# Kernel optimization log

Hardware: AMD Instinct MI355X
Metric: run time of the kernel (lower is better)

Reference implementation:

```python
import jax, jax.numpy as jnp
import numpy as np
import math

B, S, E = 4, 2048, 1024
H, KV = 16, 4            # query heads, kv heads
HD = E // H              # head_dim = 64
R, CD = 8, 64            # TPA rank, context dim
NQ, NL = 8, 2            # qubits, VQC layers
EPS = 1e-6
LN_EPS = 1e-5


def setup_inputs() -> dict:
    key = jax.random.key(0)
    ks = jax.random.split(key, 16)
    def dense(k, i, o):
        return (jax.random.normal(k, (i, o), jnp.float32) / np.float32(np.sqrt(i)))
    d = {}
    d["x"] = jax.random.normal(ks[0], (B, S, E), jnp.float32)
    d["ctxW"] = dense(ks[1], E, CD);      d["ctxb"] = jnp.zeros((CD,), jnp.float32)
    d["qaW"] = dense(ks[2], E, R * HD);   d["qab"] = jnp.zeros((R * HD,), jnp.float32)
    d["qbW"] = dense(ks[3], CD, R * H);   d["qbb"] = jnp.zeros((R * H,), jnp.float32)
    d["kaW"] = dense(ks[4], E, R * HD);   d["kab"] = jnp.zeros((R * HD,), jnp.float32)
    d["kbW"] = dense(ks[5], CD, R * KV);  d["kbb"] = jnp.zeros((R * KV,), jnp.float32)
    d["vaW"] = dense(ks[6], E, R * HD);   d["vab"] = jnp.zeros((R * HD,), jnp.float32)
    d["vbW"] = dense(ks[7], CD, R * KV);  d["vbb"] = jnp.zeros((R * KV,), jnp.float32)
    d["qeW"] = dense(ks[8], HD, NQ);      d["qeb"] = jnp.zeros((NQ,), jnp.float32)
    d["vqc"] = jax.random.normal(ks[9], (NL, NQ, 3), jnp.float32) * 0.3
    d["ent"] = jnp.array([0.1], jnp.float32)
    d["outW"] = dense(ks[10], E, E);      d["outb"] = jnp.zeros((E,), jnp.float32)
    d["gamma"] = jnp.ones((E,), jnp.float32)
    d["beta"] = jnp.zeros((E,), jnp.float32)
    return d


def _tpa(x, ctx, aW, ab, bW, bb, nh):
    # output = sum_r (x @ A_r) outer (ctx @ B_r)  ->  [b, nh, s, head_dim]
    b, s, _ = x.shape
    a = (x @ aW + ab).reshape(b, s, R, HD)
    bf = (ctx @ bW + bb).reshape(b, s, R, nh)
    return jnp.einsum('bsrd,bsrh->bhsd', a, bf)


def _quantum_features(x, qeW, qeb, vqc, ent):
    # x: [b, h, s, HD] -> features [b, h, s, 2*NQ]
    angles = jnp.tanh(x @ qeW + qeb) * math.pi
    f = angles
    for l in range(NL):
        p = vqc[l]  # [NQ, 3]
        f = jnp.cos(f + p[:, 0]) * jnp.sin(f + p[:, 1]) + jnp.cos(f + p[:, 2])
        f = f * (1.0 + ent[0] * jnp.roll(f, shift=1, axis=-1))  # entanglement
    qf = jnp.concatenate([jnp.cos(f), jnp.sin(f)], axis=-1)
    return qf / (jnp.linalg.norm(qf, axis=-1, keepdims=True) + EPS)


def reference(x, ctxW, ctxb, qaW, qab, qbW, qbb, kaW, kab, kbW, kbb,
              vaW, vab, vbW, vbb, qeW, qeb, vqc, ent, outW, outb, gamma, beta):
    ctx = x @ ctxW + ctxb                              # [B,S,CD]
    q = _tpa(x, ctx, qaW, qab, qbW, qbb, H)            # [B,H,S,HD]
    k = _tpa(x, ctx, kaW, kab, kbW, kbb, KV)           # [B,KV,S,HD]
    v = _tpa(x, ctx, vaW, vab, vbW, vbb, KV)
    # GQA: expand KV heads to match query heads
    k = jnp.repeat(k, H // KV, axis=1)
    v = jnp.repeat(v, H // KV, axis=1)
    qf = _quantum_features(q, qeW, qeb, vqc, ent)      # [B,H,S,2*NQ]
    kf = _quantum_features(k, qeW, qeb, vqc, ent)
    # causal linear attention via cumulative KV state
    kv = jnp.cumsum(jnp.einsum('bhsf,bhsd->bhsfd', kf, v), axis=2)
    num = jnp.einsum('bhsf,bhsfd->bhsd', qf, kv)
    den = jnp.einsum('bhsf,bhsf->bhs', qf, jnp.cumsum(kf, axis=2))
    attn = num / (den[..., None] + EPS)                # [B,H,S,HD]
    o = attn.transpose(0, 2, 1, 3).reshape(B, S, E) @ outW + outb
    y = x + o                                          # residual + layernorm
    mu = jnp.mean(y, axis=-1, keepdims=True)
    var = jnp.mean(jnp.square(y - mu), axis=-1, keepdims=True)
    return gamma * (y - mu) / jnp.sqrt(var + LN_EPS) + beta
```

## Files before the change

### kernel.cpp

```cpp
#include <hip/hip_runtime.h>
#include <math.h>

#define Bb  4
#define Ss  2048
#define Ee  1024
#define Hh  16
#define KVh 4
#define HD  64
#define RNK 8
#define CDd 64
#define NQ  8
#define NLn 2
#define NF  16
#define NC  32
#define CT  (Ss/NC)
#define BS  (Bb*Ss)
#define NCAT 1664

typedef unsigned short ushort_t;
typedef __attribute__((ext_vector_type(8))) short short8;
typedef __attribute__((ext_vector_type(4))) float f32x4;
typedef __attribute__((ext_vector_type(4))) unsigned short u16x4;

__device__ __forceinline__ unsigned short f2bf(float f) {
    unsigned int u = __float_as_uint(f);
    unsigned int r = (u + 0x7FFFu + ((u >> 16) & 1u)) >> 16;
    return (unsigned short)r;
}
__device__ __forceinline__ float bf2f(unsigned short h) {
    return __uint_as_float(((unsigned int)h) << 16);
}

#define GLD16(gp, lp) \
    __builtin_amdgcn_global_load_lds((const __attribute__((address_space(1))) void*)(gp), \
                                     (__attribute__((address_space(3))) void*)(lp), 16, 0, 0)

__global__ __launch_bounds__(256)
void cast_f32_bf16(const float* __restrict__ in, ushort_t* __restrict__ outp, long n)
{
    long i = ((long)blockIdx.x * blockDim.x + threadIdx.x) * 8;
    if (i >= n) return;
    short8 o;
    #pragma unroll
    for (int j = 0; j < 8; ++j) o[j] = (short)f2bf(in[i + j]);
    *(short8*)(outp + i) = o;
}

__global__ __launch_bounds__(256)
void weight_prep(const float* __restrict__ qaW, const float* __restrict__ kaW,
                 const float* __restrict__ vaW, const float* __restrict__ outW,
                 const float* __restrict__ ctxW,
                 const float* __restrict__ qab, const float* __restrict__ kab,
                 const float* __restrict__ vab, const float* __restrict__ ctxb,
                 ushort_t* __restrict__ WcatT, ushort_t* __restrict__ outWt,
                 float* __restrict__ bcat)
{
    __shared__ float t[32][33];
    const int bid = blockIdx.x;
    const int tx = threadIdx.x & 31, ty = threadIdx.x >> 5;
    if (bid < 1536) {
        const int z = bid >> 9;
        const int r = bid & 511;
        const int k0 = (r & 31) * 32, n0 = (r >> 5) * 32;
        const float* W = (z == 0) ? qaW : (z == 1) ? kaW : vaW;
        const int nOff = 512 * z;
        #pragma unroll
        for (int i = 0; i < 4; ++i)
            t[ty + 8*i][tx] = W[(size_t)(k0 + ty + 8*i) * 512 + (n0 + tx)];
        __syncthreads();
        #pragma unroll
        for (int i = 0; i < 4; ++i)
            WcatT[(size_t)(nOff + n0 + ty + 8*i) * Ee + (k0 + tx)] = f2bf(t[tx][ty + 8*i]);
    } else if (bid < 2560) {
        const int r = bid - 1536;
        const int k0 = (r & 31) * 32, n0 = (r >> 5) * 32;
        #pragma unroll
        for (int i = 0; i < 4; ++i)
            t[ty + 8*i][tx] = outW[(size_t)(k0 + ty + 8*i) * 1024 + (n0 + tx)];
        __syncthreads();
        #pragma unroll
        for (int i = 0; i < 4; ++i)
            outWt[(size_t)(n0 + ty + 8*i) * Ee + (k0 + tx)] = f2bf(t[tx][ty + 8*i]);
    } else {
        const int pid = bid - 2560;
        if (pid < 64) {
            const int k0 = (pid >> 1) * 32, n0 = (pid & 1) * 32;
            #pragma unroll
            for (int i = 0; i < 4; ++i)
                t[ty + 8*i][tx] = ctxW[(size_t)(k0 + ty + 8*i) * 64 + (n0 + tx)];
            __syncthreads();
            #pragma unroll
            for (int i = 0; i < 4; ++i)
                WcatT[(size_t)(1536 + n0 + ty + 8*i) * Ee + (k0 + tx)] = f2bf(t[tx][ty + 8*i]);
        } else if (pid < 96) {
            const int idx = (pid - 64) * 2048 + threadIdx.x * 8;
            short8 z = {0, 0, 0, 0, 0, 0, 0, 0};
            *(short8*)(WcatT + (size_t)1600 * Ee + idx) = z;
        } else {
            const int n = (pid - 96) * 256 + threadIdx.x;
            if (n < NCAT) {
                float v = 0.f;
                if      (n < 512)  v = qab[n];
                else if (n < 1024) v = kab[n - 512];
                else if (n < 1536) v = vab[n - 1024];
                else if (n < 1600) v = ctxb[n - 1536];
                bcat[n] = v;
            }
        }
    }
}

template<int RES, int OUTBF>
__global__ __launch_bounds__(256)
void gemm_mfma(const ushort_t* __restrict__ A, const ushort_t* __restrict__ Bt,
               const float* __restrict__ bias, const float* __restrict__ res,
               void* __restrict__ Cout, int M, int N, int K)
{
    __shared__ ushort_t Al[128 * 32];
    __shared__ ushort_t Bl[128 * 32];
    const int tid  = threadIdx.x;
    const int lane = tid & 63;
    const int wave = tid >> 6;
    const int wm = wave >> 1;
    const int wn = wave & 1;

    const unsigned nx  = gridDim.x;
    const unsigned bid = blockIdx.y * nx + blockIdx.x;
    const unsigned nwg = nx * gridDim.y;
    const unsigned qc = nwg >> 3, rc = nwg & 7;
    const unsigned xc = bid & 7, of = bid >> 3;
    const unsigned tile = (xc < rc ? xc * (qc + 1) : rc * (qc + 1) + (xc - rc) * qc) + of;
    const int bm = (int)(tile / nx) * 128;
    const int bn = (int)(tile % nx) * 128;

    f32x4 acc[4][4] = {};

    const int arow0 = wave * 16 + (lane >> 2);
    const int kq = lane & 3;
    const ushort_t* Ag0 = A  + (size_t)(bm + arow0) * K + kq * 8;
    const ushort_t* Ag1 = A  + (size_t)(bm + 64 + arow0) * K + kq * 8;
    const ushort_t* Bg0 = Bt + (size_t)(bn + arow0) * K + kq * 8;
    const ushort_t* Bg1 = Bt + (size_t)(bn + 64 + arow0) * K + kq * 8;
    ushort_t* Alw = Al + wave * 512;
    ushort_t* Blw = Bl + wave * 512;

    const int fr = lane & 15;
    const int fg = lane >> 4;

    for (int k0 = 0; k0 < K; k0 += 32) {
        GLD16(Ag0 + k0, Alw);
        GLD16(Ag1 + k0, Alw + 2048);
        GLD16(Bg0 + k0, Blw);
        GLD16(Bg1 + k0, Blw + 2048);
        __syncthreads();
        short8 af[4], bfv[4];
        #pragma unroll
        for (int mi = 0; mi < 4; ++mi)
            af[mi] = *(const short8*)&Al[(wm*64 + mi*16 + fr) * 32 + fg * 8];
        #pragma unroll
        for (int ni = 0; ni < 4; ++ni)
            bfv[ni] = *(const short8*)&Bl[(wn*64 + ni*16 + fr) * 32 + fg * 8];
        #pragma unroll
        for (int mi = 0; mi < 4; ++mi)
            #pragma unroll
            for (int ni = 0; ni < 4; ++ni)
                acc[mi][ni] = __builtin_amdgcn_mfma_f32_16x16x32_bf16(
                    af[mi], bfv[ni], acc[mi][ni], 0, 0, 0);
        __syncthreads();
    }

    float bv[4];
    #pragma unroll
    for (int ni = 0; ni < 4; ++ni) bv[ni] = bias[bn + wn*64 + ni*16 + fr];
    #pragma unroll
    for (int mi = 0; mi < 4; ++mi) {
        #pragma unroll
        for (int ni = 0; ni < 4; ++ni) {
            const int gn = bn + wn*64 + ni*16 + fr;
            #pragma unroll
            for (int r = 0; r < 4; ++r) {
                const int gm = bm + wm*64 + mi*16 + fg*4 + r;
                float v = acc[mi][ni][r] + bv[ni];
                if (RES) v += res[(size_t)gm * N + gn];
                if (OUTBF) ((ushort_t*)Cout)[(size_t)gm * N + gn] = f2bf(v);
                else       ((float*)Cout)[(size_t)gm * N + gn] = v;
            }
        }
    }
}

__global__ __launch_bounds__(256)
void combine_quantum(const ushort_t* __restrict__ Cf,
                     const float* __restrict__ qbW, const float* __restrict__ qbb,
                     const float* __restrict__ kbW, const float* __restrict__ kbb,
                     const float* __restrict__ vbW, const float* __restrict__ vbb,
                     const float* __restrict__ qeW, const float* __restrict__ qeb,
                     const float* __restrict__ vqc, const float* __restrict__ ent,
                     float* __restrict__ qf_g, float* __restrict__ kf_g,
                     float* __restrict__ v_g)
{
    const int wid = threadIdx.x >> 6;
    const int d   = threadIdx.x & 63;
    const int bs  = blockIdx.x * 4 + wid;
    const int b = bs >> 11;
    const int s = bs & 2047;

    __shared__ float qew_s[HD*NQ];
    __shared__ float ctx_l[4][CDd];
    __shared__ float bfq[4][128];
    __shared__ float bfk[4][32];
    __shared__ float bfv[4][32];
    __shared__ float rows[4][Hh+KVh][65];

    #pragma unroll
    for (int i = 0; i < 2; ++i)
        qew_s[threadIdx.x + 256*i] = qeW[threadIdx.x + 256*i];

    const ushort_t* Crow = Cf + (size_t)bs * NCAT;
    ctx_l[wid][d] = bf2f(Crow[1536 + d]);
    __syncthreads();

    {
        float q0 = qbb[d], q1 = qbb[d + 64];
        float kv = (d < 32) ? kbb[d] : vbb[d - 32];
        const float* Wkv = (d < 32) ? (kbW + d) : (vbW + (d - 32));
        #pragma unroll 8
        for (int k = 0; k < CDd; ++k) {
            const float c = ctx_l[wid][k];
            q0 += c * qbW[(size_t)k*128 + d];
            q1 += c * qbW[(size_t)k*128 + d + 64];
            kv += c * Wkv[(size_t)k*32];
        }
        bfq[wid][d] = q0; bfq[wid][d + 64] = q1;
        if (d < 32) bfk[wid][d] = kv; else bfv[wid][d - 32] = kv;
    }

    float aq[RNK], ak[RNK], av[RNK];
    #pragma unroll
    for (int r = 0; r < RNK; ++r) {
        aq[r] = bf2f(Crow[r*64 + d]);
        ak[r] = bf2f(Crow[512 + r*64 + d]);
        av[r] = bf2f(Crow[1024 + r*64 + d]);
    }
    __syncthreads();

    #pragma unroll
    for (int h = 0; h < Hh; ++h) {
        float acc = 0.f;
        #pragma unroll
        for (int r = 0; r < RNK; ++r) acc += aq[r] * bfq[wid][r*16 + h];
        rows[wid][h][d] = acc;
    }
    #pragma unroll
    for (int kvh = 0; kvh < KVh; ++kvh) {
        float acck = 0.f, accv = 0.f;
        #pragma unroll
        for (int r = 0; r < RNK; ++r) {
            acck += ak[r] * bfk[wid][r*4 + kvh];
            accv += av[r] * bfv[wid][r*4 + kvh];
        }
        rows[wid][Hh + kvh][d] = acck;
        v_g[((size_t)(b*KVh + kvh)*Ss + s)*HD + d] = accv;
    }
    __syncthreads();

    const float entv = ent[0];
    const int i   = d & 7;
    const int src = (d & ~7) | ((i + 7) & 7);
    float p00 = vqc[(0*NQ + i)*3 + 0], p01 = vqc[(0*NQ + i)*3 + 1], p02 = vqc[(0*NQ + i)*3 + 2];
    float p10 = vqc[(1*NQ + i)*3 + 0], p11 = vqc[(1*NQ + i)*3 + 1], p12 = vqc[(1*NQ + i)*3 + 2];
    const float qebi = qeb[i];

    #pragma unroll
    for (int stripe = 0; stripe < 3; ++stripe) {
        const int row = stripe * 8 + (d >> 3);
        const bool active = (row < Hh + KVh);
        const int rowc = active ? row : (Hh + KVh - 1);
        float acc = qebi;
        #pragma unroll 16
        for (int dd = 0; dd < HD; ++dd)
            acc += rows[wid][rowc][dd] * qew_s[dd*8 + i];
        float f = tanhf(acc) * 3.14159265358979323846f;
        float g = cosf(f + p00) * sinf(f + p01) + cosf(f + p02);
        float gp = __shfl(g, src, 64);
        f = g * (1.f + entv * gp);
        g = cosf(f + p10) * sinf(f + p11) + cosf(f + p12);
        gp = __shfl(g, src, 64);
        f = g * (1.f + entv * gp);
        float c = cosf(f), sn = sinf(f);
        float ss = c*c + sn*sn;
        ss += __shfl_xor(ss, 1, 64);
        ss += __shfl_xor(ss, 2, 64);
        ss += __shfl_xor(ss, 4, 64);
        const float inv = 1.f / (sqrtf(ss) + 1e-6f);
        if (active) {
            float* dst = (row < Hh)
                ? qf_g + ((size_t)(b*Hh + row)*Ss + s)*NF
                : kf_g + ((size_t)(b*KVh + (row - Hh))*Ss + s)*NF;
            dst[i]      = c * inv;
            dst[NQ + i] = sn * inv;
        }
    }
}

__global__ __launch_bounds__(64)
void chunk_partial(const float* __restrict__ kf_g, const float* __restrict__ v_g,
                   float* __restrict__ kvpart, float* __restrict__ kfpart)
{
    const int id = blockIdx.x;
    const int c = id & (NC-1);
    const int bk = id / NC;
    const int d = threadIdx.x;
    __shared__ float kf_l[CT][NF];
    const int s0 = c * CT;
    const float* kfp = kf_g + ((size_t)bk*Ss + s0)*NF;
    #pragma unroll
    for (int t = 0; t < (CT*NF)/64; ++t)
        ((float*)kf_l)[d + 64*t] = kfp[d + 64*t];
    __syncthreads();
    float st[NF] = {};
    const float* vp = v_g + ((size_t)bk*Ss + s0)*HD;
    for (int t = 0; t < CT; ++t) {
        const float vd = vp[(size_t)t*HD + d];
        #pragma unroll
        for (int f = 0; f < NF; ++f) st[f] += kf_l[t][f] * vd;
    }
    float* kvp = kvpart + (size_t)id * (NF*HD);
    #pragma unroll
    for (int f = 0; f < NF; ++f) kvp[f*HD + d] = st[f];
    if (d < NF) {
        float acc = 0.f;
        for (int t = 0; t < CT; ++t) acc += kf_l[t][d];
        kfpart[(size_t)id*NF + d] = acc;
    }
}

__global__ __launch_bounds__(64)
void attn_scan(const float* __restrict__ qf_g, const float* __restrict__ kf_g,
               const float* __restrict__ v_g,
               const float* __restrict__ kvpart, const float* __restrict__ kfpart,
               ushort_t* __restrict__ o_bf)
{
    const int id = blockIdx.x;
    const int c = id & (NC-1);
    const int bh = id / NC;
    const int h = bh & (Hh-1);
    const int b = bh / Hh;
    const int kvh = h >> 2;
    const int d = threadIdx.x;
    __shared__ float kf_l[CT][NF];
    __shared__ float qf_l[CT][NF];
    const int s0 = c * CT;
    const float* kfp = kf_g + ((size_t)(b*KVh + kvh)*Ss + s0)*NF;
    const float* qfp = qf_g + ((size_t)(b*Hh + h)*Ss + s0)*NF;
    #pragma unroll
    for (int t = 0; t < (CT*NF)/64; ++t) {
        ((float*)kf_l)[d + 64*t] = kfp[d + 64*t];
        ((float*)qf_l)[d + 64*t] = qfp[d + 64*t];
    }
    float st[NF] = {};
    float kfs[NF] = {};
    const int bk = b*KVh + kvh;
    for (int cc = 0; cc < c; ++cc) {
        const float* kvp = kvpart + ((size_t)bk*NC + cc)*(NF*HD);
        const float* kfq = kfpart + ((size_t)bk*NC + cc)*NF;
        #pragma unroll
        for (int f = 0; f < NF; ++f) {
            st[f]  += kvp[f*HD + d];
            kfs[f] += kfq[f];
        }
    }
    __syncthreads();
    const float* vp = v_g + ((size_t)(b*KVh + kvh)*Ss + s0)*HD;
    ushort_t* op = o_bf + ((size_t)(b*Ss + s0))*Ee + h*HD;
    for (int t = 0; t < CT; ++t) {
        const float vd = vp[(size_t)t*HD + d];
        float num0 = 0.f, num1 = 0.f, den0 = 0.f, den1 = 0.f;
        #pragma unroll
        for (int f = 0; f < NF; f += 2) {
            const float kv0 = kf_l[t][f];
            const float kv1 = kf_l[t][f+1];
            st[f]   += kv0 * vd;   kfs[f]   += kv0;
            st[f+1] += kv1 * vd;   kfs[f+1] += kv1;
            const float qv0 = qf_l[t][f];
            const float qv1 = qf_l[t][f+1];
            num0 += qv0 * st[f];   den0 += qv0 * kfs[f];
            num1 += qv1 * st[f+1]; den1 += qv1 * kfs[f+1];
        }
        op[(size_t)t*Ee + d] = f2bf((num0 + num1) / ((den0 + den1) + 1e-6f));
    }
}

__global__ __launch_bounds__(256)
void layernorm_res(const float* __restrict__ x, const ushort_t* __restrict__ o_bf,
                   const float* __restrict__ gamma, const float* __restrict__ beta,
                   float* __restrict__ out)
{
    __shared__ float tmp[4];
    const int row = blockIdx.x;
    const int t = threadIdx.x;
    const float* xp = x + (size_t)row * Ee;
    const ushort_t* op = o_bf + (size_t)row * Ee;
    const f32x4 xv = *(const f32x4*)(xp + t*4);
    const u16x4 ov = *(const u16x4*)(op + t*4);
    float v[4];
    float sum = 0.f;
    #pragma unroll
    for (int i = 0; i < 4; ++i) { v[i] = xv[i] + bf2f(ov[i]); sum += v[i]; }
    #pragma unroll
    for (int o = 32; o > 0; o >>= 1) sum += __shfl_down(sum, o, 64);
    if ((t & 63) == 0) tmp[t >> 6] = sum;
    __syncthreads();
    const float mu = (tmp[0] + tmp[1] + tmp[2] + tmp[3]) * (1.f/Ee);
    __syncthreads();
    float vs = 0.f;
    #pragma unroll
    for (int i = 0; i < 4; ++i) { const float dd = v[i] - mu; vs += dd*dd; }
    #pragma unroll
    for (int o = 32; o > 0; o >>= 1) vs += __shfl_down(vs, o, 64);
    if ((t & 63) == 0) tmp[t >> 6] = vs;
    __syncthreads();
    const float var = (tmp[0] + tmp[1] + tmp[2] + tmp[3]) * (1.f/Ee);
    const float inv = rsqrtf(var + 1e-5f);
    const f32x4 gv = *(const f32x4*)(gamma + t*4);
    const f32x4 bv = *(const f32x4*)(beta + t*4);
    f32x4 ovec;
    #pragma unroll
    for (int i = 0; i < 4; ++i) ovec[i] = gv[i] * (v[i] - mu) * inv + bv[i];
    *(f32x4*)(out + (size_t)row * Ee + t*4) = ovec;
}

extern "C" void kernel_launch(void* const* d_in, const int* in_sizes, int n_in,
                              void* d_out, int out_size, void* d_ws, size_t ws_size,
                              hipStream_t stream)
{
    const float* x    = (const float*)d_in[0];
    const float* ctxW = (const float*)d_in[1];
    const float* ctxb = (const float*)d_in[2];
    const float* qaW  = (const float*)d_in[3];
    const float* qab  = (const float*)d_in[4];
    const float* qbW  = (const float*)d_in[5];
    const float* qbb  = (const float*)d_in[6];
    const float* kaW  = (const float*)d_in[7];
    const float* kab  = (const float*)d_in[8];
    const float* kbW  = (const float*)d_in[9];
    const float* kbb  = (const float*)d_in[10];
    const float* vaW  = (const float*)d_in[11];
    const float* vab  = (const float*)d_in[12];
    const float* vbW  = (const float*)d_in[13];
    const float* vbb  = (const float*)d_in[14];
    const float* qeW  = (const float*)d_in[15];
    const float* qeb  = (const float*)d_in[16];
    const float* vqc  = (const float*)d_in[17];
    const float* ent  = (const float*)d_in[18];
    const float* outW = (const float*)d_in[19];
    const float* outb = (const float*)d_in[20];
    const float* gamma= (const float*)d_in[21];
    const float* beta = (const float*)d_in[22];
    float* out = (float*)d_out;

    char* p = (char*)d_ws;
    auto alloc = [&](size_t bytes) { char* r = p; p += (bytes + 255) & ~(size_t)255; return (void*)r; };
    ushort_t* xb    = (ushort_t*)alloc((size_t)BS * Ee * 2);
    ushort_t* WcatT = (ushort_t*)alloc((size_t)NCAT * Ee * 2);
    ushort_t* outWt = (ushort_t*)alloc((size_t)Ee * Ee * 2);
    float*    bcat  = (float*)   alloc(NCAT * 4);
    ushort_t* Cf    = (ushort_t*)alloc((size_t)BS * NCAT * 2);
    float*    qf    = (float*)   alloc((size_t)Bb*Hh*Ss*NF * 4);
    float*    kf    = (float*)   alloc((size_t)Bb*KVh*Ss*NF * 4);
    float*    vg    = (float*)   alloc((size_t)Bb*KVh*Ss*HD * 4);
    float*    kvpart= (float*)   alloc((size_t)Bb*KVh*NC*NF*HD * 4);
    float*    kfpart= (float*)   alloc((size_t)Bb*KVh*NC*NF * 4);
    ushort_t* obf   = Cf;
    ushort_t* obf2  = (ushort_t*)qf;

    cast_f32_bf16<<<(BS*(long)Ee/8 + 255)/256, 256, 0, stream>>>(x, xb, (long)BS*Ee);
    weight_prep<<<2663, 256, 0, stream>>>(qaW, kaW, vaW, outW, ctxW,
                                          qab, kab, vab, ctxb, WcatT, outWt, bcat);

    gemm_mfma<0,1><<<dim3(NCAT/128, BS/128), 256, 0, stream>>>(
        xb, WcatT, bcat, nullptr, Cf, BS, NCAT, Ee);
    combine_quantum<<<BS/4, 256, 0, stream>>>(Cf, qbW, qbb, kbW, kbb, vbW, vbb,
                                              qeW, qeb, vqc, ent, qf, kf, vg);
    chunk_partial<<<Bb*KVh*NC, 64, 0, stream>>>(kf, vg, kvpart, kfpart);
    attn_scan<<<Bb*Hh*NC, 64, 0, stream>>>(qf, kf, vg, kvpart, kfpart, obf);
    gemm_mfma<0,1><<<dim3(Ee/128, BS/128), 256, 0, stream>>>(
        obf, outWt, outb, nullptr, obf2, BS, Ee, Ee);
    layernorm_res<<<BS, 256, 0, stream>>>(x, obf2, gamma, beta, out);
}
```

Measured before the change: 303.6 us.

## Add chunk prefix-scan kernel, double chunk count, merge prep kernels, share ctx weight loads

A separate prefix_scan kernel turns per-chunk KV partial states into exclusive prefixes. Each attn_scan block then loads one prefix instead of summing all earlier chunks, which removes work that grew with chunk index. The chunk count is doubled to 64, giving more blocks and shorter serial loops per chunk. The x cast and weight prep are merged into one launch, and the small ctx-projection is restructured so each weight element is loaded once and used for all four rows in the block. The cost is an extra small serial-over-chunks kernel launch.

```diff
diff --git a/kernel.cpp b/kernel.cpp
--- a/kernel.cpp
+++ b/kernel.cpp
@@ -12,7 +12,7 @@
 #define NQ  8
 #define NLn 2
 #define NF  16
-#define NC  32
+#define NC  64
 #define CT  (Ss/NC)
 #define BS  (Bb*Ss)
 #define NCAT 1664
@@ -36,31 +36,28 @@
                                      (__attribute__((address_space(3))) void*)(lp), 16, 0, 0)
 
 __global__ __launch_bounds__(256)
-void cast_f32_bf16(const float* __restrict__ in, ushort_t* __restrict__ outp, long n)
-{
-    long i = ((long)blockIdx.x * blockDim.x + threadIdx.x) * 8;
-    if (i >= n) return;
-    short8 o;
-    #pragma unroll
-    for (int j = 0; j < 8; ++j) o[j] = (short)f2bf(in[i + j]);
-    *(short8*)(outp + i) = o;
-}
-
-__global__ __launch_bounds__(256)
-void weight_prep(const float* __restrict__ qaW, const float* __restrict__ kaW,
-                 const float* __restrict__ vaW, const float* __restrict__ outW,
-                 const float* __restrict__ ctxW,
-                 const float* __restrict__ qab, const float* __restrict__ kab,
-                 const float* __restrict__ vab, const float* __restrict__ ctxb,
-                 ushort_t* __restrict__ WcatT, ushort_t* __restrict__ outWt,
-                 float* __restrict__ bcat)
+void prep_all(const float* __restrict__ x, ushort_t* __restrict__ xb,
+              const float* __restrict__ qaW, const float* __restrict__ kaW,
+              const float* __restrict__ vaW, const float* __restrict__ outW,
+              const float* __restrict__ ctxW,
+              const float* __restrict__ qab, const float* __restrict__ kab,
+              const float* __restrict__ vab, const float* __restrict__ ctxb,
+              ushort_t* __restrict__ WcatT, ushort_t* __restrict__ outWt,
+              float* __restrict__ bcat)
 {
     __shared__ float t[32][33];
     const int bid = blockIdx.x;
     const int tx = threadIdx.x & 31, ty = threadIdx.x >> 5;
-    if (bid < 1536) {
-        const int z = bid >> 9;
-        const int r = bid & 511;
+    if (bid < 4096) {
+        const long i = (long)bid * 2048 + threadIdx.x * 8;
+        short8 o;
+        #pragma unroll
+        for (int j = 0; j < 8; ++j) o[j] = (short)f2bf(x[i + j]);
+        *(short8*)(xb + i) = o;
+    } else if (bid < 5632) {
+        const int r0 = bid - 4096;
+        const int z = r0 >> 9;
+        const int r = r0 & 511;
         const int k0 = (r & 31) * 32, n0 = (r >> 5) * 32;
         const float* W = (z == 0) ? qaW : (z == 1) ? kaW : vaW;
         const int nOff = 512 * z;
@@ -71,8 +68,8 @@
         #pragma unroll
         for (int i = 0; i < 4; ++i)
             WcatT[(size_t)(nOff + n0 + ty + 8*i) * Ee + (k0 + tx)] = f2bf(t[tx][ty + 8*i]);
-    } else if (bid < 2560) {
-        const int r = bid - 1536;
+    } else if (bid < 6656) {
+        const int r = bid - 5632;
         const int k0 = (r & 31) * 32, n0 = (r >> 5) * 32;
         #pragma unroll
         for (int i = 0; i < 4; ++i)
@@ -82,7 +79,7 @@
         for (int i = 0; i < 4; ++i)
             outWt[(size_t)(n0 + ty + 8*i) * Ee + (k0 + tx)] = f2bf(t[tx][ty + 8*i]);
     } else {
-        const int pid = bid - 2560;
+        const int pid = bid - 6656;
         if (pid < 64) {
             const int k0 = (pid >> 1) * 32, n0 = (pid & 1) * 32;
             #pragma unroll
@@ -221,18 +218,31 @@
     __syncthreads();
 
     {
-        float q0 = qbb[d], q1 = qbb[d + 64];
-        float kv = (d < 32) ? kbb[d] : vbb[d - 32];
-        const float* Wkv = (d < 32) ? (kbW + d) : (vbW + (d - 32));
-        #pragma unroll 8
-        for (int k = 0; k < CDd; ++k) {
-            const float c = ctx_l[wid][k];
-            q0 += c * qbW[(size_t)k*128 + d];
-            q1 += c * qbW[(size_t)k*128 + d + 64];
-            kv += c * Wkv[(size_t)k*32];
-        }
-        bfq[wid][d] = q0; bfq[wid][d + 64] = q1;
-        if (d < 32) bfk[wid][d] = kv; else bfv[wid][d - 32] = kv;
+        const int t = threadIdx.x;
+        if (t < 192) {
+            const float* Wc; float bb; int ldw;
+            if (t < 128)      { Wc = qbW + t;         bb = qbb[t];       ldw = 128; }
+            else if (t < 160) { Wc = kbW + (t - 128); bb = kbb[t - 128]; ldw = 32;  }
+            else              { Wc = vbW + (t - 160); bb = vbb[t - 160]; ldw = 32;  }
+            float a0 = bb, a1 = bb, a2 = bb, a3 = bb;
+            #pragma unroll 8
+            for (int k = 0; k < CDd; ++k) {
+                const float w = Wc[(size_t)k * ldw];
+                a0 += ctx_l[0][k] * w;
+                a1 += ctx_l[1][k] * w;
+                a2 += ctx_l[2][k] * w;
+                a3 += ctx_l[3][k] * w;
+            }
+            if (t < 128) {
+                bfq[0][t] = a0; bfq[1][t] = a1; bfq[2][t] = a2; bfq[3][t] = a3;
+            } else if (t < 160) {
+                const int n = t - 128;
+                bfk[0][n] = a0; bfk[1][n] = a1; bfk[2][n] = a2; bfk[3][n] = a3;
+            } else {
+                const int n = t - 160;
+                bfv[0][n] = a0; bfv[1][n] = a1; bfv[2][n] = a2; bfv[3][n] = a3;
+            }
+        }
     }
 
     float aq[RNK], ak[RNK], av[RNK];
@@ -335,6 +345,33 @@
     }
 }
 
+__global__ void prefix_scan(float* __restrict__ kvpart, float* __restrict__ kfpart)
+{
+    const int idx = blockIdx.x * blockDim.x + threadIdx.x;
+    const int total = Bb*KVh * (NF*HD + NF);
+    if (idx >= total) return;
+    const int bk = idx / (NF*HD + NF);
+    const int e = idx % (NF*HD + NF);
+    if (e < NF*HD) {
+        float* p = kvpart + (size_t)bk*NC*(NF*HD) + e;
+        float run = 0.f;
+        for (int c = 0; c < NC; ++c) {
+            const float t = p[(size_t)c*(NF*HD)];
+            p[(size_t)c*(NF*HD)] = run;
+            run += t;
+        }
+    } else {
+        const int f = e - NF*HD;
+        float* p = kfpart + (size_t)bk*NC*NF + f;
+        float run = 0.f;
+        for (int c = 0; c < NC; ++c) {
+            const float t = p[(size_t)c*NF];
+            p[(size_t)c*NF] = run;
+            run += t;
+        }
+    }
+}
+
 __global__ __launch_bounds__(64)
 void attn_scan(const float* __restrict__ qf_g, const float* __restrict__ kf_g,
                const float* __restrict__ v_g,
@@ -358,18 +395,11 @@
         ((float*)kf_l)[d + 64*t] = kfp[d + 64*t];
         ((float*)qf_l)[d + 64*t] = qfp[d + 64*t];
     }
-    float st[NF] = {};
-    float kfs[NF] = {};
-    const int bk = b*KVh + kvh;
-    for (int cc = 0; cc < c; ++cc) {
-        const float* kvp = kvpart + ((size_t)bk*NC + cc)*(NF*HD);
-        const float* kfq = kfpart + ((size_t)bk*NC + cc)*NF;
-        #pragma unroll
-        for (int f = 0; f < NF; ++f) {
-            st[f]  += kvp[f*HD + d];
-            kfs[f] += kfq[f];
-        }
-    }
+    float st[NF], kfs[NF];
+    const float* kvp  = kvpart + ((size_t)(b*KVh + kvh)*NC + c)*(NF*HD);
+    const float* kfsp = kfpart + ((size_t)(b*KVh + kvh)*NC + c)*NF;
+    #pragma unroll
+    for (int f = 0; f < NF; ++f) { st[f] = kvp[f*HD + d]; kfs[f] = kfsp[f]; }
     __syncthreads();
     const float* vp = v_g + ((size_t)(b*KVh + kvh)*Ss + s0)*HD;
     ushort_t* op = o_bf + ((size_t)(b*Ss + s0))*Ee + h*HD;
@@ -474,15 +504,15 @@
     ushort_t* obf   = Cf;
     ushort_t* obf2  = (ushort_t*)qf;
 
-    cast_f32_bf16<<<(BS*(long)Ee/8 + 255)/256, 256, 0, stream>>>(x, xb, (long)BS*Ee);
-    weight_prep<<<2663, 256, 0, stream>>>(qaW, kaW, vaW, outW, ctxW,
-                                          qab, kab, vab, ctxb, WcatT, outWt, bcat);
+    prep_all<<<6759, 256, 0, stream>>>(x, xb, qaW, kaW, vaW, outW, ctxW,
+                                       qab, kab, vab, ctxb, WcatT, outWt, bcat);
 
     gemm_mfma<0,1><<<dim3(NCAT/128, BS/128), 256, 0, stream>>>(
         xb, WcatT, bcat, nullptr, Cf, BS, NCAT, Ee);
     combine_quantum<<<BS/4, 256, 0, stream>>>(Cf, qbW, qbb, kbW, kbb, vbW, vbb,
                                               qeW, qeb, vqc, ent, qf, kf, vg);
     chunk_partial<<<Bb*KVh*NC, 64, 0, stream>>>(kf, vg, kvpart, kfpart);
+    prefix_scan<<<(Bb*KVh*(NF*HD + NF) + 255)/256, 256, 0, stream>>>(kvpart, kfpart);
     attn_scan<<<Bb*Hh*NC, 64, 0, stream>>>(qf, kf, vg, kvpart, kfpart, obf);
     gemm_mfma<0,1><<<dim3(Ee/128, BS/128), 256, 0, stream>>>(
         obf, outWt, outb, nullptr, obf2, BS, Ee, Ee);
```

Result: faster. 289.0 us (-4.8%).
